# Performance work log

Hardware: AMD Instinct MI355X
Metric: run time of the kernel (lower is better)

## Reference

```python
import jax, jax.numpy as jnp
import numpy as np

B, L, D, H, FF, K = 2, 2048, 1024, 16, 4096, 5
HD = D // H
EPS = 1e-5

def _rope_matrix():
    pos = jnp.arange(L, dtype=jnp.float32)
    inv = 1.0 / (10000.0 ** (jnp.arange(0, HD, 2, dtype=jnp.float32) / HD))
    ang = pos[:, None] * inv[None, :]                       # [L, HD//2]
    # buffer layout matches torch: cat([cos, sin], -1) -> [1,1,L,HD]
    return jnp.concatenate([jnp.cos(ang), jnp.sin(ang)], -1)[None, None]

def _alibi():
    i = jnp.arange(L)
    dist = jnp.clip(i[:, None] - i[None, :], 0, None).astype(jnp.float32)
    slopes = 2.0 ** (-(2.0 ** (-(np.log2(H) - 3.0))) * jnp.arange(H, dtype=jnp.float32))
    return slopes[:, None, None] * dist                     # [H,L,L]

def _apply_rope(x, pe):
    # faithful even/odd slicing of the concatenated [cos|sin] buffer
    xe, xo = x[..., ::2], x[..., 1::2]
    c, s = pe[..., ::2], pe[..., 1::2]
    return jnp.concatenate([xe * c - xo * s, xe * s + xo * c], -1)

def _ln(x, g, b):
    m = x.mean(-1, keepdims=True)
    v = ((x - m) ** 2).mean(-1, keepdims=True)
    return (x - m) * jax.lax.rsqrt(v + EPS) * g + b

def _attn(x, wq, bq, wk, bk, wv, bv, wo, bo, pe, alibi):
    q = (x @ wq + bq).reshape(B, L, H, HD).transpose(0, 2, 1, 3)
    k = (x @ wk + bk).reshape(B, L, H, HD).transpose(0, 2, 1, 3)
    v = (x @ wv + bv).reshape(B, L, H, HD).transpose(0, 2, 1, 3)
    q = _apply_rope(q, pe)
    k = _apply_rope(k, pe)
    scores = jnp.einsum('bhqd,bhkd->bhqk', q, k) * (HD ** -0.5) + alibi[None]
    w = jax.nn.softmax(scores, axis=-1)
    o = jnp.einsum('bhqk,bhkd->bhqd', w, v).transpose(0, 2, 1, 3).reshape(B, L, D)
    return o @ wo + bo

def _conv_block(x, g, b, pw1_w, pw1_b, dw_w, dw_b, bn_g, bn_b, pw2_w, pw2_b):
    res = x
    h = _ln(x, g, b)
    h = h @ pw1_w + pw1_b                                   # pointwise 1: [B,L,2D]
    h = h[..., :D] * jax.nn.sigmoid(h[..., D:])             # GLU -> [B,L,D]
    h = h.transpose(0, 2, 1)                                # [B,D,L]
    w = dw_w[:, None, ::-1]                                 # ConvTranspose1d(stride=1,pad=K//2) == corr with flipped kernel
    h = jax.lax.conv_general_dilated(h, w, (1,), [(K // 2, K // 2)],
        dimension_numbers=('NCH', 'OIH', 'NCH'), feature_group_count=D)
    h = h + dw_b[None, :, None]
    h = h * jax.lax.rsqrt(jnp.float32(1.0 + EPS)) * bn_g[None, :, None] + bn_b[None, :, None]  # eval BN
    h = h * jax.nn.relu6(h + 3.0) / 6.0                     # hardswish
    h = h.transpose(0, 2, 1) @ pw2_w + pw2_b                # pointwise 2: [B,L,D]
    return h + res[:, :1, :]                                # Upsample(size=1) residual (nearest -> t=0)

def reference(memory, wq, bq, wk, bk, wv, bv, wo, bo, n1_g, n1_b,
              cln_g, cln_b, pw1_w, pw1_b, dw_w, dw_b, bn_g, bn_b, pw2_w, pw2_b,
              proj_w, proj_b, proj2_w, proj2_b, lin1_w, lin1_b, lin2_w, lin2_b,
              n3_g, n3_b):
    pe = _rope_matrix()
    alibi = _alibi()
    tgt2 = _attn(memory, wq, bq, wk, bk, wv, bv, wo, bo, pe, alibi)
    memory = memory + _ln(tgt2, n1_g, n1_b)
    conv = _conv_block(memory, cln_g, cln_b, pw1_w, pw1_b, dw_w, dw_b,
                       bn_g, bn_b, pw2_w, pw2_b)
    proj = jnp.einsum('bld,lm->bmd', memory, proj_w) + proj_b[:, None]   # Linear over seq axis
    proj = proj @ proj2_w + proj2_b
    memory = proj + conv
    tgt2 = jax.nn.gelu(memory @ lin1_w + lin1_b, approximate=False) @ lin2_w + lin2_b
    return _ln(memory + tgt2, n3_g, n3_b)

def setup_inputs():
    ks = iter(jax.random.split(jax.random.key(0), 48))
    def w(shape, s=0.02):
        return jax.random.normal(next(ks), shape, dtype=jnp.float32) * s
    z = lambda *s: jnp.zeros(s, dtype=jnp.float32)
    o = lambda *s: jnp.ones(s, dtype=jnp.float32)
    return {
        'memory': jax.random.normal(next(ks), (B, L, D), dtype=jnp.float32),
        'wq': w((D, D)), 'bq': z(D), 'wk': w((D, D)), 'bk': z(D),
        'wv': w((D, D)), 'bv': z(D), 'wo': w((D, D)), 'bo': z(D),
        'n1_g': o(D), 'n1_b': z(D),
        'cln_g': o(D), 'cln_b': z(D),
        'pw1_w': w((D, 2 * D)), 'pw1_b': z(2 * D),
        'dw_w': w((D, K), 0.1), 'dw_b': z(D),
        'bn_g': o(D), 'bn_b': z(D),
        'pw2_w': w((D, D)), 'pw2_b': z(D),
        'proj_w': w((L, L)), 'proj_b': z(L),
        'proj2_w': w((D, D)), 'proj2_b': z(D),
        'lin1_w': w((D, FF)), 'lin1_b': z(FF),
        'lin2_w': w((FF, D)), 'lin2_b': z(D),
        'n3_g': o(D), 'n3_b': z(D),
    }
```

## Files before the change

kernel.cpp:

```cpp
#include <hip/hip_runtime.h>
#include <hip/hip_bf16.h>
#include <math.h>

constexpr int Bc = 2, Lc = 2048, Dc = 1024, Hc = 16, HDc = 64, FFc = 4096;
constexpr int NT = Bc * Lc;
constexpr size_t TD = (size_t)NT * Dc;
constexpr size_t MEG = 1024 * 1024;

__device__ __forceinline__ float ldf(const float* p) { return *p; }
__device__ __forceinline__ unsigned short f2b(float f) {
  __hip_bfloat16 h = __float2bfloat16(f);
  return *reinterpret_cast<unsigned short*>(&h);
}

using frag   = __attribute__((ext_vector_type(8))) short;
using f32x4v = __attribute__((ext_vector_type(4))) float;

__device__ __forceinline__ void async16(const unsigned short* g, unsigned short* l) {
  __builtin_amdgcn_global_load_lds(
      (const __attribute__((address_space(1))) unsigned int*)g,
      (__attribute__((address_space(3))) unsigned int*)l, 16, 0, 0);
}

__device__ __forceinline__ float block_sum(float v, float* red) {
  const int lane = threadIdx.x & 63, w = threadIdx.x >> 6;
  #pragma unroll
  for (int o = 32; o > 0; o >>= 1) v += __shfl_down(v, o, 64);
  __syncthreads();
  if (lane == 0) red[w] = v;
  __syncthreads();
  return red[0] + red[1] + red[2] + red[3];
}

__global__ __launch_bounds__(256)
void convert_bf16_kernel(const float* __restrict__ IN, unsigned short* __restrict__ OUT)
{
  const size_t gid = (size_t)blockIdx.x * 256 + threadIdx.x;
  const float4 v = *(const float4*)(IN + gid * 4);
  ushort4 o;
  o.x = f2b(v.x); o.y = f2b(v.y); o.z = f2b(v.z); o.w = f2b(v.w);
  *(ushort4*)(OUT + gid * 4) = o;
}

__global__ __launch_bounds__(256)
void transpose_convert_kernel(const float* __restrict__ IN, unsigned short* __restrict__ OUT,
                              int R, int C, long long sIn, long long sOut)
{
  __shared__ float tile[64][65];
  const int t = threadIdx.x;
  const float* in = IN + (long long)blockIdx.z * sIn;
  unsigned short* out = OUT + (long long)blockIdx.z * sOut;
  const int r0 = blockIdx.y * 64, c0 = blockIdx.x * 64;
  #pragma unroll
  for (int i = 0; i < 4; i++) {
    const int r = (t >> 4) + i * 16, c4 = (t & 15) * 4;
    const float4 v = *(const float4*)(in + (size_t)(r0 + r) * C + c0 + c4);
    tile[r][c4+0] = v.x; tile[r][c4+1] = v.y; tile[r][c4+2] = v.z; tile[r][c4+3] = v.w;
  }
  __syncthreads();
  #pragma unroll
  for (int i = 0; i < 4; i++) {
    const int cc = (t >> 4) + i * 16, rr4 = (t & 15) * 4;
    ushort4 o;
    o.x = f2b(tile[rr4+0][cc]); o.y = f2b(tile[rr4+1][cc]);
    o.z = f2b(tile[rr4+2][cc]); o.w = f2b(tile[rr4+3][cc]);
    *(ushort4*)(out + (size_t)(c0 + cc) * R + r0 + rr4) = o;
  }
}

struct TPack {
  const float* in[10]; unsigned short* out[10];
  int R[10], C[10], tx[10], start[10];
};
__global__ __launch_bounds__(256)
void fused_transpose_kernel(TPack p)
{
  __shared__ float tile[64][65];
  const int bid = blockIdx.x;
  int s = 0;
  #pragma unroll
  for (int i = 1; i < 10; i++) s = (bid >= p.start[i]) ? i : s;
  const float* in = p.in[s];
  unsigned short* out = p.out[s];
  const int R = p.R[s], C = p.C[s];
  const int local = bid - p.start[s];
  const int bx = local % p.tx[s], by = local / p.tx[s];
  const int r0 = by * 64, c0 = bx * 64;
  const int t = threadIdx.x;
  #pragma unroll
  for (int i = 0; i < 4; i++) {
    const int r = (t >> 4) + i * 16, c4 = (t & 15) * 4;
    const float4 v = *(const float4*)(in + (size_t)(r0 + r) * C + c0 + c4);
    tile[r][c4+0] = v.x; tile[r][c4+1] = v.y; tile[r][c4+2] = v.z; tile[r][c4+3] = v.w;
  }
  __syncthreads();
  #pragma unroll
  for (int i = 0; i < 4; i++) {
    const int cc = (t >> 4) + i * 16, rr4 = (t & 15) * 4;
    ushort4 o;
    o.x = f2b(tile[rr4+0][cc]); o.y = f2b(tile[rr4+1][cc]);
    o.z = f2b(tile[rr4+2][cc]); o.w = f2b(tile[rr4+3][cc]);
    *(ushort4*)(out + (size_t)(c0 + cc) * R + r0 + rr4) = o;
  }
}

constexpr int EPI_BIAS = 0, EPI_BIAS_ROW = 1, EPI_GELU = 2, EPI_ADD = 3, EPI_ADDROW0 = 4,
              EPI_QKV = 5;

template<int BM, int EPI, bool OUTBF, bool OUTBOTH>
__global__ __launch_bounds__(256)
void mfma_gemm_kernel(const unsigned short* __restrict__ A, const unsigned short* __restrict__ Bt,
                      const float* __restrict__ bias, const float* __restrict__ bias2,
                      const float* __restrict__ bias3, const float* __restrict__ extra,
                      float* __restrict__ C, unsigned short* __restrict__ Cbf,
                      int M, int N, int K,
                      long long sA, long long sB, long long sC)
{
  constexpr int NTt = (BM == 128) ? 4 : 2;
  __shared__ unsigned short As[BM][4][8];
  __shared__ unsigned short Bs[128][4][8];
  const int tid = threadIdx.x;
  const int l = tid & 63, w = tid >> 6;
  const int wm = (BM == 128) ? (w & 1) * 64 : 0;
  const int wn = (BM == 128) ? (w >> 1) * 64 : w * 32;
  const int m0 = blockIdx.y * BM, n0 = blockIdx.x * 128;
  const unsigned short* Ap = A + (long long)blockIdx.z * sA;
  const unsigned short* Bp = Bt + (long long)blockIdx.z * sB;

  f32x4v acc[4][NTt];
  #pragma unroll
  for (int mt = 0; mt < 4; mt++)
    #pragma unroll
    for (int nt = 0; nt < NTt; nt++) acc[mt][nt] = {0.f, 0.f, 0.f, 0.f};

  const int c_ = l >> 4, rm = l & 15;
  int rrB[2], ggB[2];
  #pragma unroll
  for (int j = 0; j < 2; j++) {
    const int chunk = w * 128 + j * 64 + l;
    rrB[j] = chunk >> 2;
    ggB[j] = (chunk & 3) ^ (rrB[j] & 3);
  }
  int rrA = 0, ggA = 0;
  if constexpr (BM == 64) {
    const int chunkA = w * 64 + l;
    rrA = chunkA >> 2;
    ggA = (chunkA & 3) ^ (rrA & 3);
  }

  for (int k0 = 0; k0 < K; k0 += 32) {
    __syncthreads();
    if constexpr (BM == 128) {
      #pragma unroll
      for (int j = 0; j < 2; j++) {
        async16(Ap + (size_t)(m0 + rrB[j]) * K + k0 + ggB[j] * 8,
                &As[0][0][0] + (size_t)(w * 128 + j * 64) * 8);
        async16(Bp + (size_t)(n0 + rrB[j]) * K + k0 + ggB[j] * 8,
                &Bs[0][0][0] + (size_t)(w * 128 + j * 64) * 8);
      }
    } else {
      async16(Ap + (size_t)(m0 + rrA) * K + k0 + ggA * 8,
              &As[0][0][0] + (size_t)(w * 64) * 8);
      #pragma unroll
      for (int j = 0; j < 2; j++)
        async16(Bp + (size_t)(n0 + rrB[j]) * K + k0 + ggB[j] * 8,
                &Bs[0][0][0] + (size_t)(w * 128 + j * 64) * 8);
    }
    __syncthreads();

    frag af[4], bfr[NTt];
    #pragma unroll
    for (int mt = 0; mt < 4; mt++)
      af[mt] = *(const frag*)&As[wm + mt * 16 + rm][c_ ^ (rm & 3)][0];
    #pragma unroll
    for (int nt = 0; nt < NTt; nt++)
      bfr[nt] = *(const frag*)&Bs[wn + nt * 16 + rm][c_ ^ (rm & 3)][0];
    #pragma unroll
    for (int mt = 0; mt < 4; mt++)
      #pragma unroll
      for (int nt = 0; nt < NTt; nt++)
        acc[mt][nt] = __builtin_amdgcn_mfma_f32_16x16x32_bf16(af[mt], bfr[nt], acc[mt][nt], 0, 0, 0);
  }

  float* Cp = C + (long long)blockIdx.z * sC;
  unsigned short* Cbp = Cbf + (long long)blockIdx.z * sC;
  #pragma unroll
  for (int mt = 0; mt < 4; mt++) {
    #pragma unroll
    for (int nt = 0; nt < NTt; nt++) {
      const int mq = m0 + wm + mt * 16 + c_ * 4;
      const int n  = n0 + wn + nt * 16 + rm;
      if constexpr (EPI == EPI_QKV) {
        const float* bp = (n < 1024) ? bias : ((n < 2048) ? bias2 : bias3);
        const float bv_ = ldf(bp + (n & 1023));
        const float r0 = acc[mt][nt][0] + bv_;
        const float r1 = acc[mt][nt][1] + bv_;
        const float r2 = acc[mt][nt][2] + bv_;
        const float r3 = acc[mt][nt][3] + bv_;
        if (n < 2048) {
          float* dst = Cp + (size_t)(n >> 10) * TD + (size_t)mq * Dc + (n & 1023);
          dst[0] = r0; dst[Dc] = r1; dst[2 * Dc] = r2; dst[3 * Dc] = r3;
        } else {
          ushort4 o;
          o.x = f2b(r0); o.y = f2b(r1); o.z = f2b(r2); o.w = f2b(r3);
          *(ushort4*)(Cbp + (size_t)(mq >> 11) * ((size_t)Lc * Dc)
                      + (size_t)(n - 2048) * Lc + (mq & (Lc - 1))) = o;
        }
      } else {
        #pragma unroll
        for (int i = 0; i < 4; i++) {
          const int m = mq + i;
          float r = acc[mt][nt][i];
          if constexpr (EPI == EPI_BIAS || EPI == EPI_GELU || EPI == EPI_ADD || EPI == EPI_ADDROW0)
            r += ldf(bias + n);
          if constexpr (EPI == EPI_BIAS_ROW) r += ldf(bias + m);
          if constexpr (EPI == EPI_GELU)
            r = 0.5f * r * (1.0f + erff(r * 0.70710678118654752f));
          if constexpr (EPI == EPI_ADD) r += extra[(size_t)m * N + n];
          if constexpr (EPI == EPI_ADDROW0) r += extra[(size_t)(m >> 11) * ((size_t)Lc * Dc) + n];
          if constexpr (OUTBOTH) { Cp[(size_t)m * N + n] = r; Cbp[(size_t)m * N + n] = f2b(r); }
          else if constexpr (OUTBF) Cbp[(size_t)m * N + n] = f2b(r);
          else                      Cp[(size_t)m * N + n] = r;
        }
      }
    }
  }
}

__global__ __launch_bounds__(256)
void pe_fill_kernel(float* __restrict__ pet)
{
  const int gid = blockIdx.x * 256 + threadIdx.x;
  const int l = gid >> 6, t = gid & 63;
  const int j = t & 31;
  const float wj = exp2f(-(float)j * (13.2877123795494f / 32.0f));
  const float ang = (float)l * wj;
  pet[gid] = (t < 32) ? cosf(ang) : sinf(ang);
}

__global__ __launch_bounds__(256)
void rope2_kernel(const float* __restrict__ Qi, const float* __restrict__ Ki,
                  const float* __restrict__ pet,
                  unsigned short* __restrict__ Qo, unsigned short* __restrict__ Ko)
{
  int gid = blockIdx.x * 256 + threadIdx.x;
  const int sel = gid >= NT * Hc;
  if (sel) gid -= NT * Hc;
  const float* X = sel ? Ki : Qi;
  unsigned short* O = sel ? Ko : Qo;
  const int h = gid & (Hc - 1);
  const int token = gid >> 4;
  const int l = token & (Lc - 1);
  const float* p = X + (size_t)token * Dc + h * HDc;
  unsigned short* po = O + (size_t)token * Dc + h * HDc;
  const float* pr = pet + l * 64;
  float x[64], out[64];
  #pragma unroll
  for (int i = 0; i < 16; i++) *(float4*)&x[4*i] = *(const float4*)&p[4*i];
  #pragma unroll
  for (int u = 0; u < 32; u++) {
    const int base = (u < 16) ? (2 * u) : (32 + 2 * (u - 16));
    const float c = pr[base], s = pr[base + 1];
    out[u]      = x[2*u] * c - x[2*u+1] * s;
    out[32 + u] = x[2*u] * s + x[2*u+1] * c;
  }
  #pragma unroll
  for (int i = 0; i < 16; i++) {
    ushort4 o;
    o.x = f2b(out[4*i+0]); o.y = f2b(out[4*i+1]);
    o.z = f2b(out[4*i+2]); o.w = f2b(out[4*i+3]);
    *(ushort4*)&po[4*i] = o;
  }
}

__global__ __launch_bounds__(256)
void flash_attn_mfma_kernel(const unsigned short* __restrict__ Q,
                            const unsigned short* __restrict__ K,
                            const unsigned short* __restrict__ VT,
                            unsigned short* __restrict__ O)
{
  __shared__ unsigned short Qs[128][8][8];
  __shared__ unsigned short Ks[64][8][8];
  __shared__ unsigned short Vt[64][8][8];
  __shared__ unsigned short Ps[128][72];
  const int tid = threadIdx.x;
  const int l = tid & 63, w = tid >> 6;
  const int lg = l >> 4, lm = l & 15;
  const int q0 = blockIdx.x * 128;
  const int bh = blockIdx.y;
  const int b = bh >> 4, h = bh & 15;
  const size_t rowbase = (size_t)b * Lc;
  const size_t vbase = (size_t)b * Lc * Dc;
  const int dbase = h * 64;
  const float sc1 = 0.125f * 1.44269504f;
  const float sl2 = exp2f(-0.5f * (float)h) * 1.44269504f;

  #pragma unroll
  for (int j = 0; j < 4; j++) {
    const int chunk = (w * 4 + j) * 64 + l;
    const int r = chunk >> 3, gsrc = (chunk & 7) ^ (r & 7);
    async16(Q + (rowbase + q0 + r) * Dc + dbase + gsrc * 8,
            &Qs[0][0][0] + (size_t)chunk * 8);
  }
  __syncthreads();
  frag qf[2][2];
  #pragma unroll
  for (int qt = 0; qt < 2; qt++)
    #pragma unroll
    for (int s = 0; s < 2; s++)
      qf[qt][s] = *(const frag*)&Qs[w * 32 + qt * 16 + lm][(s * 4 + lg) ^ (lm & 7)][0];

  float m_i[2], l_i[2];
  f32x4v acc_o[2][4];
  #pragma unroll
  for (int qt = 0; qt < 2; qt++) {
    m_i[qt] = -3.0e38f; l_i[qt] = 0.f;
    #pragma unroll
    for (int dt = 0; dt < 4; dt++) acc_o[qt][dt] = {0.f, 0.f, 0.f, 0.f};
  }

  for (int k0 = 0; k0 < Lc; k0 += 64) {
    __syncthreads();
    #pragma unroll
    for (int j = 0; j < 2; j++) {
      const int chunk = (w * 2 + j) * 64 + l;
      const int r = chunk >> 3, gsrc = (chunk & 7) ^ (r & 7);
      async16(K + (rowbase + k0 + r) * Dc + dbase + gsrc * 8,
              &Ks[0][0][0] + (size_t)chunk * 8);
      async16(VT + vbase + (size_t)(dbase + r) * Lc + k0 + gsrc * 8,
              &Vt[0][0][0] + (size_t)chunk * 8);
    }
    __syncthreads();

    f32x4v st[2][4];
    #pragma unroll
    for (int qt = 0; qt < 2; qt++)
      #pragma unroll
      for (int kt = 0; kt < 4; kt++) st[qt][kt] = {0.f, 0.f, 0.f, 0.f};
    #pragma unroll
    for (int kt = 0; kt < 4; kt++) {
      #pragma unroll
      for (int s = 0; s < 2; s++) {
        frag kf = *(const frag*)&Ks[kt * 16 + lm][(s * 4 + lg) ^ (lm & 7)][0];
        #pragma unroll
        for (int qt = 0; qt < 2; qt++)
          st[qt][kt] = __builtin_amdgcn_mfma_f32_16x16x32_bf16(kf, qf[qt][s], st[qt][kt], 0, 0, 0);
      }
    }

    #pragma unroll
    for (int qt = 0; qt < 2; qt++) {
      const float qg = (float)(q0 + w * 32 + qt * 16 + lm);
      float sv[4][4], tmax = -3.0e38f;
      #pragma unroll
      for (int kt = 0; kt < 4; kt++)
        #pragma unroll
        for (int i = 0; i < 4; i++) {
          const float kg = (float)(k0 + kt * 16 + lg * 4 + i);
          const float v = st[qt][kt][i] * sc1 + sl2 * fmaxf(qg - kg, 0.0f);
          sv[kt][i] = v; tmax = fmaxf(tmax, v);
        }
      tmax = fmaxf(tmax, __shfl_xor(tmax, 16, 64));
      tmax = fmaxf(tmax, __shfl_xor(tmax, 32, 64));
      const float mnew = fmaxf(m_i[qt], tmax);
      const float alpha = exp2f(m_i[qt] - mnew);
      m_i[qt] = mnew;
      float rsum = 0.f;
      const int qrow = w * 32 + qt * 16 + lm;
      #pragma unroll
      for (int kt = 0; kt < 4; kt++) {
        const float p0 = exp2f(sv[kt][0] - mnew), p1 = exp2f(sv[kt][1] - mnew);
        const float p2 = exp2f(sv[kt][2] - mnew), p3 = exp2f(sv[kt][3] - mnew);
        rsum += (p0 + p1) + (p2 + p3);
        ushort4 pk4;
        pk4.x = f2b(p0); pk4.y = f2b(p1); pk4.z = f2b(p2); pk4.w = f2b(p3);
        *(ushort4*)&Ps[qrow][kt * 16 + lg * 4] = pk4;
      }
      rsum += __shfl_xor(rsum, 16, 64);
      rsum += __shfl_xor(rsum, 32, 64);
      l_i[qt] = l_i[qt] * alpha + rsum;
      float aO[4];
      #pragma unroll
      for (int i = 0; i < 4; i++) aO[i] = __shfl(alpha, lg * 4 + i, 64);
      #pragma unroll
      for (int dt = 0; dt < 4; dt++)
        #pragma unroll
        for (int i = 0; i < 4; i++) acc_o[qt][dt][i] *= aO[i];
    }

    #pragma unroll
    for (int c = 0; c < 2; c++) {
      frag ap[2];
      #pragma unroll
      for (int qt = 0; qt < 2; qt++)
        ap[qt] = *(const frag*)&Ps[w * 32 + qt * 16 + lm][c * 32 + lg * 8];
      #pragma unroll
      for (int dt = 0; dt < 4; dt++) {
        frag bv = *(const frag*)&Vt[dt * 16 + lm][(c * 4 + lg) ^ (lm & 7)][0];
        #pragma unroll
        for (int qt = 0; qt < 2; qt++)
          acc_o[qt][dt] = __builtin_amdgcn_mfma_f32_16x16x32_bf16(ap[qt], bv, acc_o[qt][dt], 0, 0, 0);
      }
    }
  }

  #pragma unroll
  for (int qt = 0; qt < 2; qt++) {
    float lO[4];
    #pragma unroll
    for (int i = 0; i < 4; i++) lO[i] = 1.0f / __shfl(l_i[qt], lg * 4 + i, 64);
    #pragma unroll
    for (int dt = 0; dt < 4; dt++)
      #pragma unroll
      for (int i = 0; i < 4; i++)
        Ps[w * 32 + qt * 16 + lg * 4 + i][dt * 16 + lm] = f2b(acc_o[qt][dt][i] * lO[i]);
  }
  __syncthreads();
  #pragma unroll
  for (int j = 0; j < 4; j++) {
    const int chunk = (w * 4 + j) * 64 + l;
    const int r = chunk >> 3, g = chunk & 7;
    alignas(16) unsigned short tmp[8];
    #pragma unroll
    for (int t = 0; t < 8; t++) tmp[t] = Ps[r][g * 8 + t];
    *(uint4*)(O + (rowbase + q0 + r) * Dc + dbase + g * 8) = *(uint4*)tmp;
  }
}

__global__ __launch_bounds__(256)
void ln_res_cln_kernel(const float* __restrict__ X, const float* __restrict__ RES,
                       const float* __restrict__ g1, const float* __restrict__ b1,
                       const float* __restrict__ g2, const float* __restrict__ b2,
                       float* __restrict__ OUT1, unsigned short* __restrict__ OUT2)
{
  __shared__ float red4[4];
  const int row = blockIdx.x, tid = threadIdx.x;
  const size_t base = (size_t)row * Dc + tid * 4;
  const float4 xv = *(const float4*)(X + base);
  float s = xv.x + xv.y + xv.z + xv.w;
  s = block_sum(s, red4);
  const float mean = s * (1.0f / Dc);
  const float d0 = xv.x-mean, d1 = xv.y-mean, d2 = xv.z-mean, d3 = xv.w-mean;
  float ss = d0*d0 + d1*d1 + d2*d2 + d3*d3;
  ss = block_sum(ss, red4);
  const float rstd = rsqrtf(ss * (1.0f / Dc) + 1e-5f);
  const int c = tid * 4;
  const float4 rv = *(const float4*)(RES + base);
  float y0 = rv.x + d0*rstd*ldf(g1+c+0) + ldf(b1+c+0);
  float y1 = rv.y + d1*rstd*ldf(g1+c+1) + ldf(b1+c+1);
  float y2 = rv.z + d2*rstd*ldf(g1+c+2) + ldf(b1+c+2);
  float y3 = rv.w + d3*rstd*ldf(g1+c+3) + ldf(b1+c+3);
  *(float4*)(OUT1 + base) = make_float4(y0, y1, y2, y3);
  float s2 = y0 + y1 + y2 + y3;
  s2 = block_sum(s2, red4);
  const float mean2 = s2 * (1.0f / Dc);
  const float e0 = y0-mean2, e1 = y1-mean2, e2 = y2-mean2, e3 = y3-mean2;
  float ss2 = e0*e0 + e1*e1 + e2*e2 + e3*e3;
  ss2 = block_sum(ss2, red4);
  const float rstd2 = rsqrtf(ss2 * (1.0f / Dc) + 1e-5f);
  ushort4 o;
  o.x = f2b(e0*rstd2*ldf(g2+c+0) + ldf(b2+c+0));
  o.y = f2b(e1*rstd2*ldf(g2+c+1) + ldf(b2+c+1));
  o.z = f2b(e2*rstd2*ldf(g2+c+2) + ldf(b2+c+2));
  o.w = f2b(e3*rstd2*ldf(g2+c+3) + ldf(b2+c+3));
  *(ushort4*)(OUT2 + base) = o;
}

__global__ __launch_bounds__(256)
void ln_sum_kernel(const float* __restrict__ X, const float* __restrict__ Y,
                   const float* __restrict__ g, const float* __restrict__ be,
                   float* __restrict__ OUT)
{
  __shared__ float red4[4];
  const int row = blockIdx.x, tid = threadIdx.x;
  const size_t base = (size_t)row * Dc + tid * 4;
  const float4 xv = *(const float4*)(X + base);
  const float4 yv = *(const float4*)(Y + base);
  const float x0 = xv.x+yv.x, x1 = xv.y+yv.y, x2 = xv.z+yv.z, x3 = xv.w+yv.w;
  float s = x0 + x1 + x2 + x3;
  s = block_sum(s, red4);
  const float mean = s * (1.0f / Dc);
  const float d0 = x0-mean, d1 = x1-mean, d2 = x2-mean, d3 = x3-mean;
  float ss = d0*d0 + d1*d1 + d2*d2 + d3*d3;
  ss = block_sum(ss, red4);
  const float rstd = rsqrtf(ss * (1.0f / Dc) + 1e-5f);
  const int c = tid * 4;
  float4 o;
  o.x = d0*rstd*ldf(g+c+0) + ldf(be+c+0);
  o.y = d1*rstd*ldf(g+c+1) + ldf(be+c+1);
  o.z = d2*rstd*ldf(g+c+2) + ldf(be+c+2);
  o.w = d3*rstd*ldf(g+c+3) + ldf(be+c+3);
  *(float4*)(OUT + base) = o;
}

__global__ __launch_bounds__(256)
void glu_kernel(const float* __restrict__ H1, float* __restrict__ HG)
{
  const int gid = blockIdx.x * 256 + threadIdx.x;
  const int t = gid >> 8;
  const int c4 = (gid & 255) * 4;
  const float* p = H1 + (size_t)t * (2 * Dc);
  const float4 a = *(const float4*)(p + c4);
  const float4 gg = *(const float4*)(p + Dc + c4);
  float4 o;
  o.x = a.x / (1.0f + expf(-gg.x));
  o.y = a.y / (1.0f + expf(-gg.y));
  o.z = a.z / (1.0f + expf(-gg.z));
  o.w = a.w / (1.0f + expf(-gg.w));
  *(float4*)(HG + (size_t)t * Dc + c4) = o;
}

__global__ __launch_bounds__(256)
void dwconv_bf16_kernel(const float* __restrict__ HG, const float* __restrict__ w,
                        const float* __restrict__ wb, const float* __restrict__ gn,
                        const float* __restrict__ bb, unsigned short* __restrict__ OUT)
{
  const int gid = blockIdx.x * 256 + threadIdx.x;
  const int d = gid & (Dc - 1);
  const int l = (gid >> 10) & (Lc - 1);
  const int b = gid >> 21;
  const size_t rowb = (size_t)b * Lc;
  float acc = ldf(wb + d);
  #pragma unroll
  for (int s = 0; s < 5; s++) {
    const int lp = l + 2 - s;
    if (lp >= 0 && lp < Lc)
      acc += ldf(w + d * 5 + s) * HG[((rowb + lp) << 10) + d];
  }
  const float rs = rsqrtf(1.0f + 1e-5f);
  const float t = acc * rs * ldf(gn + d) + ldf(bb + d);
  OUT[gid] = f2b(t * fminf(fmaxf(t + 3.0f, 0.0f), 6.0f) * (1.0f / 6.0f));
}

extern "C" void kernel_launch(void* const* d_in, const int* in_sizes, int n_in,
                              void* d_out, int out_size, void* d_ws, size_t ws_size,
                              hipStream_t stream) {
  (void)in_sizes; (void)n_in; (void)out_size; (void)ws_size;
  const float* mem    = (const float*)d_in[0];
  const float* wq     = (const float*)d_in[1];
  const float* bq     = (const float*)d_in[2];
  const float* wk     = (const float*)d_in[3];
  const float* bk     = (const float*)d_in[4];
  const float* wv     = (const float*)d_in[5];
  const float* bv     = (const float*)d_in[6];
  const float* wo     = (const float*)d_in[7];
  const float* bo     = (const float*)d_in[8];
  const float* n1g    = (const float*)d_in[9];
  const float* n1b    = (const float*)d_in[10];
  const float* clng   = (const float*)d_in[11];
  const float* clnb   = (const float*)d_in[12];
  const float* pw1w   = (const float*)d_in[13];
  const float* pw1b   = (const float*)d_in[14];
  const float* dww    = (const float*)d_in[15];
  const float* dwb    = (const float*)d_in[16];
  const float* bng    = (const float*)d_in[17];
  const float* bnb    = (const float*)d_in[18];
  const float* pw2w   = (const float*)d_in[19];
  const float* pw2b   = (const float*)d_in[20];
  const float* projw  = (const float*)d_in[21];
  const float* projb  = (const float*)d_in[22];
  const float* proj2w = (const float*)d_in[23];
  const float* proj2b = (const float*)d_in[24];
  const float* lin1w  = (const float*)d_in[25];
  const float* lin1b  = (const float*)d_in[26];
  const float* lin2w  = (const float*)d_in[27];
  const float* lin2b  = (const float*)d_in[28];
  const float* n3g    = (const float*)d_in[29];
  const float* n3b    = (const float*)d_in[30];
  float* out = (float*)d_out;

  char* base = (char*)d_ws;
  float* qb   = (float*)base;
  float* kb   = qb + TD;
  float* big1 = kb + TD;
  float* big2 = big1 + TD;
  float* ob   = big2 + TD;
  unsigned short* abf  = (unsigned short*)(base + 5 * TD * 4);
  unsigned short* qbf  = abf + TD;
  unsigned short* kbf  = qbf + TD;
  unsigned short* vtb  = kbf + TD;
  unsigned short* m1T  = vtb + TD;
  unsigned short* ffbbf= m1T + TD;
  unsigned short* wt   = ffbbf + 4 * TD;
  unsigned short* wqT    = wt;
  unsigned short* wkT    = wqT + MEG;
  unsigned short* wvT    = wkT + MEG;
  unsigned short* woT    = wvT + MEG;
  unsigned short* pw1T   = woT + MEG;
  unsigned short* pw2T   = pw1T + 2*MEG;
  unsigned short* proj2T = pw2T + MEG;
  unsigned short* projwT = proj2T + MEG;
  unsigned short* lin1T  = projwT + 4*MEG;
  unsigned short* lin2T  = lin1T + 4*MEG;
  float* pet = (float*)(lin2T + 4*MEG);

  const dim3 blk(256);
  const long long LD = (long long)Lc * Dc;

  TPack tp;
  const float* tin[10]  = {wq, wk, wv, wo, pw1w, pw2w, proj2w, projw, lin1w, lin2w};
  unsigned short* tout[10] = {wqT, wkT, wvT, woT, pw1T, pw2T, proj2T, projwT, lin1T, lin2T};
  const int tR[10] = {1024,1024,1024,1024,1024,1024,1024,2048,1024,4096};
  const int tC[10] = {1024,1024,1024,1024,2048,1024,1024,2048,4096,1024};
  int startAcc = 0;
  for (int i = 0; i < 10; i++) {
    tp.in[i] = tin[i]; tp.out[i] = tout[i];
    tp.R[i] = tR[i]; tp.C[i] = tC[i]; tp.tx[i] = tC[i] / 64;
    tp.start[i] = startAcc;
    startAcc += (tR[i] / 64) * (tC[i] / 64);
  }
  fused_transpose_kernel<<<dim3(startAcc), blk, 0, stream>>>(tp);
  pe_fill_kernel<<<dim3(Lc * 64 / 256), blk, 0, stream>>>(pet);

  convert_bf16_kernel<<<dim3((unsigned)(TD/1024)),blk,0,stream>>>(mem, abf);
  mfma_gemm_kernel<128,EPI_QKV,false,false><<<dim3(24,32,1),blk,0,stream>>>(
      abf, wqT, bq, bk, bv, nullptr, qb, vtb, NT, 3*Dc, Dc, 0, 0, 0);
  rope2_kernel<<<dim3(2*NT*Hc/256),blk,0,stream>>>(qb, kb, pet, qbf, kbf);
  flash_attn_mfma_kernel<<<dim3(Lc/128, Bc*Hc),blk,0,stream>>>(qbf,kbf,vtb,abf);
  mfma_gemm_kernel<64,EPI_BIAS,false,false><<<dim3(8,64,1),blk,0,stream>>>(
      abf,woT,bo,nullptr,nullptr,nullptr,qb,nullptr,NT,Dc,Dc,0,0,0);
  ln_res_cln_kernel<<<dim3(NT),blk,0,stream>>>(qb, mem, n1g, n1b, clng, clnb, kb, abf);

  mfma_gemm_kernel<128,EPI_BIAS,false,false><<<dim3(16,32,1),blk,0,stream>>>(
      abf,pw1T,pw1b,nullptr,nullptr,nullptr,big1,nullptr,NT,2*Dc,Dc,0,0,0);
  glu_kernel<<<dim3((unsigned)(TD/4/256)),blk,0,stream>>>(big1, ob);
  dwconv_bf16_kernel<<<dim3((unsigned)(TD/256)),blk,0,stream>>>(ob, dww, dwb, bng, bnb, abf);
  mfma_gemm_kernel<64,EPI_ADDROW0,false,false><<<dim3(8,64,1),blk,0,stream>>>(
      abf,pw2T,pw2b,nullptr,nullptr,kb,big2,nullptr,NT,Dc,Dc,0,0,0);

  transpose_convert_kernel<<<dim3(16,32,2),blk,0,stream>>>(kb, m1T, 2048, 1024, LD, LD);
  mfma_gemm_kernel<64,EPI_BIAS_ROW,true,false><<<dim3(8,32,2),blk,0,stream>>>(
      projwT,m1T,projb,nullptr,nullptr,nullptr,nullptr,abf,Lc,Dc,Lc,0,LD,LD);
  mfma_gemm_kernel<64,EPI_ADD,false,true><<<dim3(8,64,1),blk,0,stream>>>(
      abf,proj2T,proj2b,nullptr,nullptr,big2,big1,qbf,NT,Dc,Dc,0,0,0);

  mfma_gemm_kernel<128,EPI_GELU,true,false><<<dim3(32,32,1),blk,0,stream>>>(
      qbf,lin1T,lin1b,nullptr,nullptr,nullptr,nullptr,ffbbf,NT,FFc,Dc,0,0,0);
  mfma_gemm_kernel<64,EPI_BIAS,false,false><<<dim3(8,64,1),blk,0,stream>>>(
      ffbbf,lin2T,lin2b,nullptr,nullptr,nullptr,ob,nullptr,NT,Dc,FFc,0,0,0);

  ln_sum_kernel<<<dim3(NT),blk,0,stream>>>(big1, ob, n3g, n3b, out);
}
```

Measured before the change: 726.5 us.

## Halve flash-attention query tile, add lazy rescale and MFMA priority hints

The attention kernel now gives each block 64 query rows instead of 128, so each wave owns one 16-row tile and the grid doubles to 1024 blocks. This is meant to raise occupancy and cut register pressure. It also skips the output rescale when no row max in the wave grew, and raises wave priority around the MFMA sections with s_setprio. The cost is that K/V tiles are loaded from global memory twice as often per query row, and each tile load now feeds half as much MFMA work.

```diff
diff --git a/kernel.cpp b/kernel.cpp
--- a/kernel.cpp
+++ b/kernel.cpp
@@ -279,14 +279,14 @@
                             const unsigned short* __restrict__ VT,
                             unsigned short* __restrict__ O)
 {
-  __shared__ unsigned short Qs[128][8][8];
+  __shared__ unsigned short Qs[64][8][8];
   __shared__ unsigned short Ks[64][8][8];
   __shared__ unsigned short Vt[64][8][8];
-  __shared__ unsigned short Ps[128][72];
+  __shared__ unsigned short Ps[64][72];
   const int tid = threadIdx.x;
   const int l = tid & 63, w = tid >> 6;
   const int lg = l >> 4, lm = l & 15;
-  const int q0 = blockIdx.x * 128;
+  const int q0 = blockIdx.x * 64;
   const int bh = blockIdx.y;
   const int b = bh >> 4, h = bh & 15;
   const size_t rowbase = (size_t)b * Lc;
@@ -296,28 +296,22 @@
   const float sl2 = exp2f(-0.5f * (float)h) * 1.44269504f;
 
   #pragma unroll
-  for (int j = 0; j < 4; j++) {
-    const int chunk = (w * 4 + j) * 64 + l;
+  for (int j = 0; j < 2; j++) {
+    const int chunk = (w * 2 + j) * 64 + l;
     const int r = chunk >> 3, gsrc = (chunk & 7) ^ (r & 7);
     async16(Q + (rowbase + q0 + r) * Dc + dbase + gsrc * 8,
             &Qs[0][0][0] + (size_t)chunk * 8);
   }
   __syncthreads();
-  frag qf[2][2];
-  #pragma unroll
-  for (int qt = 0; qt < 2; qt++)
-    #pragma unroll
-    for (int s = 0; s < 2; s++)
-      qf[qt][s] = *(const frag*)&Qs[w * 32 + qt * 16 + lm][(s * 4 + lg) ^ (lm & 7)][0];
-
-  float m_i[2], l_i[2];
-  f32x4v acc_o[2][4];
-  #pragma unroll
-  for (int qt = 0; qt < 2; qt++) {
-    m_i[qt] = -3.0e38f; l_i[qt] = 0.f;
-    #pragma unroll
-    for (int dt = 0; dt < 4; dt++) acc_o[qt][dt] = {0.f, 0.f, 0.f, 0.f};
-  }
+  frag qf[2];
+  #pragma unroll
+  for (int s = 0; s < 2; s++)
+    qf[s] = *(const frag*)&Qs[w * 16 + lm][(s * 4 + lg) ^ (lm & 7)][0];
+
+  float m_i = -3.0e38f, l_i = 0.f;
+  f32x4v acc_o[4];
+  #pragma unroll
+  for (int dt = 0; dt < 4; dt++) acc_o[dt] = {0.f, 0.f, 0.f, 0.f};
 
   for (int k0 = 0; k0 < Lc; k0 += 64) {
     __syncthreads();
@@ -332,93 +326,85 @@
     }
     __syncthreads();
 
-    f32x4v st[2][4];
-    #pragma unroll
-    for (int qt = 0; qt < 2; qt++)
-      #pragma unroll
-      for (int kt = 0; kt < 4; kt++) st[qt][kt] = {0.f, 0.f, 0.f, 0.f};
+    f32x4v st[4];
+    #pragma unroll
+    for (int kt = 0; kt < 4; kt++) st[kt] = {0.f, 0.f, 0.f, 0.f};
+    __builtin_amdgcn_s_setprio(1);
     #pragma unroll
     for (int kt = 0; kt < 4; kt++) {
       #pragma unroll
       for (int s = 0; s < 2; s++) {
         frag kf = *(const frag*)&Ks[kt * 16 + lm][(s * 4 + lg) ^ (lm & 7)][0];
-        #pragma unroll
-        for (int qt = 0; qt < 2; qt++)
-          st[qt][kt] = __builtin_amdgcn_mfma_f32_16x16x32_bf16(kf, qf[qt][s], st[qt][kt], 0, 0, 0);
+        st[kt] = __builtin_amdgcn_mfma_f32_16x16x32_bf16(kf, qf[s], st[kt], 0, 0, 0);
       }
     }
-
-    #pragma unroll
-    for (int qt = 0; qt < 2; qt++) {
-      const float qg = (float)(q0 + w * 32 + qt * 16 + lm);
-      float sv[4][4], tmax = -3.0e38f;
-      #pragma unroll
-      for (int kt = 0; kt < 4; kt++)
-        #pragma unroll
-        for (int i = 0; i < 4; i++) {
-          const float kg = (float)(k0 + kt * 16 + lg * 4 + i);
-          const float v = st[qt][kt][i] * sc1 + sl2 * fmaxf(qg - kg, 0.0f);
-          sv[kt][i] = v; tmax = fmaxf(tmax, v);
-        }
-      tmax = fmaxf(tmax, __shfl_xor(tmax, 16, 64));
-      tmax = fmaxf(tmax, __shfl_xor(tmax, 32, 64));
-      const float mnew = fmaxf(m_i[qt], tmax);
-      const float alpha = exp2f(m_i[qt] - mnew);
-      m_i[qt] = mnew;
-      float rsum = 0.f;
-      const int qrow = w * 32 + qt * 16 + lm;
-      #pragma unroll
-      for (int kt = 0; kt < 4; kt++) {
-        const float p0 = exp2f(sv[kt][0] - mnew), p1 = exp2f(sv[kt][1] - mnew);
-        const float p2 = exp2f(sv[kt][2] - mnew), p3 = exp2f(sv[kt][3] - mnew);
-        rsum += (p0 + p1) + (p2 + p3);
-        ushort4 pk4;
-        pk4.x = f2b(p0); pk4.y = f2b(p1); pk4.z = f2b(p2); pk4.w = f2b(p3);
-        *(ushort4*)&Ps[qrow][kt * 16 + lg * 4] = pk4;
+    __builtin_amdgcn_s_setprio(0);
+
+    const float qg = (float)(q0 + w * 16 + lm);
+    float sv[4][4], tmax = -3.0e38f;
+    #pragma unroll
+    for (int kt = 0; kt < 4; kt++)
+      #pragma unroll
+      for (int i = 0; i < 4; i++) {
+        const float kg = (float)(k0 + kt * 16 + lg * 4 + i);
+        const float v = st[kt][i] * sc1 + sl2 * fmaxf(qg - kg, 0.0f);
+        sv[kt][i] = v; tmax = fmaxf(tmax, v);
       }
-      rsum += __shfl_xor(rsum, 16, 64);
-      rsum += __shfl_xor(rsum, 32, 64);
-      l_i[qt] = l_i[qt] * alpha + rsum;
+    tmax = fmaxf(tmax, __shfl_xor(tmax, 16, 64));
+    tmax = fmaxf(tmax, __shfl_xor(tmax, 32, 64));
+    if (__any(tmax > m_i)) {
+      const float mnew = fmaxf(m_i, tmax);
+      const float alpha = exp2f(m_i - mnew);
+      m_i = mnew;
+      l_i *= alpha;
       float aO[4];
       #pragma unroll
       for (int i = 0; i < 4; i++) aO[i] = __shfl(alpha, lg * 4 + i, 64);
       #pragma unroll
       for (int dt = 0; dt < 4; dt++)
         #pragma unroll
-        for (int i = 0; i < 4; i++) acc_o[qt][dt][i] *= aO[i];
+        for (int i = 0; i < 4; i++) acc_o[dt][i] *= aO[i];
     }
-
+    float rsum = 0.f;
+    const int qrow = w * 16 + lm;
+    #pragma unroll
+    for (int kt = 0; kt < 4; kt++) {
+      const float p0 = exp2f(sv[kt][0] - m_i), p1 = exp2f(sv[kt][1] - m_i);
+      const float p2 = exp2f(sv[kt][2] - m_i), p3 = exp2f(sv[kt][3] - m_i);
+      rsum += (p0 + p1) + (p2 + p3);
+      ushort4 pk4;
+      pk4.x = f2b(p0); pk4.y = f2b(p1); pk4.z = f2b(p2); pk4.w = f2b(p3);
+      *(ushort4*)&Ps[qrow][kt * 16 + lg * 4] = pk4;
+    }
+    rsum += __shfl_xor(rsum, 16, 64);
+    rsum += __shfl_xor(rsum, 32, 64);
+    l_i += rsum;
+
+    __builtin_amdgcn_s_setprio(1);
     #pragma unroll
     for (int c = 0; c < 2; c++) {
-      frag ap[2];
-      #pragma unroll
-      for (int qt = 0; qt < 2; qt++)
-        ap[qt] = *(const frag*)&Ps[w * 32 + qt * 16 + lm][c * 32 + lg * 8];
+      frag ap = *(const frag*)&Ps[w * 16 + lm][c * 32 + lg * 8];
       #pragma unroll
       for (int dt = 0; dt < 4; dt++) {
         frag bv = *(const frag*)&Vt[dt * 16 + lm][(c * 4 + lg) ^ (lm & 7)][0];
-        #pragma unroll
-        for (int qt = 0; qt < 2; qt++)
-          acc_o[qt][dt] = __builtin_amdgcn_mfma_f32_16x16x32_bf16(ap[qt], bv, acc_o[qt][dt], 0, 0, 0);
+        acc_o[dt] = __builtin_amdgcn_mfma_f32_16x16x32_bf16(ap, bv, acc_o[dt], 0, 0, 0);
       }
     }
-  }
-
-  #pragma unroll
-  for (int qt = 0; qt < 2; qt++) {
-    float lO[4];
-    #pragma unroll
-    for (int i = 0; i < 4; i++) lO[i] = 1.0f / __shfl(l_i[qt], lg * 4 + i, 64);
-    #pragma unroll
-    for (int dt = 0; dt < 4; dt++)
-      #pragma unroll
-      for (int i = 0; i < 4; i++)
-        Ps[w * 32 + qt * 16 + lg * 4 + i][dt * 16 + lm] = f2b(acc_o[qt][dt][i] * lO[i]);
-  }
+    __builtin_amdgcn_s_setprio(0);
+  }
+
+  float lO[4];
+  #pragma unroll
+  for (int i = 0; i < 4; i++) lO[i] = 1.0f / __shfl(l_i, lg * 4 + i, 64);
+  #pragma unroll
+  for (int dt = 0; dt < 4; dt++)
+    #pragma unroll
+    for (int i = 0; i < 4; i++)
+      Ps[w * 16 + lg * 4 + i][dt * 16 + lm] = f2b(acc_o[dt][i] * lO[i]);
   __syncthreads();
   #pragma unroll
-  for (int j = 0; j < 4; j++) {
-    const int chunk = (w * 4 + j) * 64 + l;
+  for (int j = 0; j < 2; j++) {
+    const int chunk = (w * 2 + j) * 64 + l;
     const int r = chunk >> 3, g = chunk & 7;
     alignas(16) unsigned short tmp[8];
     #pragma unroll
@@ -616,7 +602,7 @@
   mfma_gemm_kernel<128,EPI_QKV,false,false><<<dim3(24,32,1),blk,0,stream>>>(
       abf, wqT, bq, bk, bv, nullptr, qb, vtb, NT, 3*Dc, Dc, 0, 0, 0);
   rope2_kernel<<<dim3(2*NT*Hc/256),blk,0,stream>>>(qb, kb, pet, qbf, kbf);
-  flash_attn_mfma_kernel<<<dim3(Lc/128, Bc*Hc),blk,0,stream>>>(qbf,kbf,vtb,abf);
+  flash_attn_mfma_kernel<<<dim3(Lc/64, Bc*Hc),blk,0,stream>>>(qbf,kbf,vtb,abf);
   mfma_gemm_kernel<64,EPI_BIAS,false,false><<<dim3(8,64,1),blk,0,stream>>>(
       abf,woT,bo,nullptr,nullptr,nullptr,qb,nullptr,NT,Dc,Dc,0,0,0);
   ln_res_cln_kernel<<<dim3(NT),blk,0,stream>>>(qb, mem, n1g, n1b, clng, clnb, kb, abf);
```

Measured after the change: 701.1 us. 3.5% less time.
